# Optimization experiments

Measured on AMD Instinct MI355X. Metric: run time of the kernel, lower is better.

## Reference

```python
import jax, jax.numpy as jnp
import numpy as np

B, T, D, H, NHASH, BS, L, DFF = 4, 4096, 512, 8, 4, 64, 4, 2048
DH = D // H           # 64
NB = T // BS          # 64 buckets per hash round
MASK_VAL = -5e4       # TOKEN_SELF_ATTN_VALUE from reformer-pytorch


def setup_inputs() -> dict:
    key = jax.random.key(0)
    ks = jax.random.split(key, 8)
    s = D ** -0.5
    return {
        "src": jax.random.normal(ks[0], (B, T, D), jnp.float32),
        "rotations": jax.random.normal(ks[1], (L, DH, NHASH, NB // 2), jnp.float32),
        "Wqk": jax.random.normal(ks[2], (L, D, D), jnp.float32) * s,
        "Wv": jax.random.normal(ks[3], (L, D, D), jnp.float32) * s,
        "Wout": jax.random.normal(ks[4], (L, D, D), jnp.float32) * s,
        "bout": jnp.zeros((L, D), jnp.float32),
        "W1": jax.random.normal(ks[5], (L, DFF, D), jnp.float32) * s,
        "b1": jnp.zeros((L, DFF), jnp.float32),
        "W2": jax.random.normal(ks[6], (L, D, DFF), jnp.float32) * (DFF ** -0.5),
        "b2": jnp.zeros((L, D), jnp.float32),
        "g2": jnp.ones((L, D), jnp.float32),
        "be2": jnp.zeros((L, D), jnp.float32),
        "gf": jnp.ones((D,), jnp.float32),
        "bf": jnp.zeros((D,), jnp.float32),
    }


def _ln(x, g, b, eps=1e-6):
    m = x.mean(-1, keepdims=True)
    v = ((x - m) ** 2).mean(-1, keepdims=True)
    return (x - m) * jax.lax.rsqrt(v + eps) * g + b


def _look_one_back(x):
    # concat each chunk with the previous chunk along the within-chunk axis
    return jnp.concatenate([x, jnp.roll(x, 1, axis=1)], axis=2)


def _lsh_attention(qk, v, rot):
    # qk, v: (bh, T, DH); rot: (DH, NHASH, NB//2). Shared-QK LSH attention.
    bh = qk.shape[0]
    rotated = jnp.einsum('btf,fhr->bhtr', qk, rot)               # (bh,NHASH,T,NB/2)
    full = jnp.concatenate([rotated, -rotated], axis=-1)          # (bh,NHASH,T,NB)
    buckets = jnp.argmax(full, axis=-1)                           # (bh,NHASH,T)
    buckets = buckets + (jnp.arange(NHASH) * NB)[None, :, None]   # offset per round
    buckets = buckets.reshape(bh, NHASH * T)

    ticker = jnp.arange(NHASH * T)
    bt = buckets * T + (ticker % T)                               # unique sort keys
    sticker = jnp.argsort(bt, axis=-1)                            # sort positions
    undo = jnp.argsort(sticker, axis=-1)
    st = sticker % T                                              # original positions

    sqk = jnp.take_along_axis(qk, st[..., None], axis=1)          # (bh,NHASH*T,DH)
    sv = jnp.take_along_axis(v, st[..., None], axis=1)

    C = NHASH * NB                                                # chunks
    bq_t = st.reshape(bh, C, BS)
    bqk = sqk.reshape(bh, C, BS, DH)
    bv = sv.reshape(bh, C, BS, DH)

    bq = bqk
    bk = bqk / jnp.maximum(jnp.linalg.norm(bqk, axis=-1, keepdims=True), 1e-12)
    bk = _look_one_back(bk)                                       # (bh,C,2*BS,DH)
    bv = _look_one_back(bv)
    bkv_t = _look_one_back(bq_t)                                  # (bh,C,2*BS)

    dots = jnp.einsum('bcie,bcje->bcij', bq, bk) * (DH ** -0.5)   # (bh,C,BS,2BS)
    self_mask = bq_t[:, :, :, None] == bkv_t[:, :, None, :]
    dots = jnp.where(self_mask, MASK_VAL, dots)

    lse = jax.scipy.special.logsumexp(dots, axis=-1, keepdims=True)
    probs = jnp.exp(dots - lse)
    bo = jnp.einsum('bcij,bcje->bcie', probs, bv)                 # (bh,C,BS,DH)

    so = bo.reshape(bh, NHASH * T, DH)
    slog = lse.reshape(bh, NHASH * T)
    o = jnp.take_along_axis(so, undo[..., None], axis=1).reshape(bh, NHASH, T, DH)
    lg = jnp.take_along_axis(slog, undo, axis=1).reshape(bh, NHASH, T, 1)
    w = jnp.exp(lg - jax.scipy.special.logsumexp(lg, axis=1, keepdims=True))
    return jnp.sum(o * w, axis=1)                                 # (bh,T,DH)


def _split_heads(x):
    return x.reshape(B, T, H, DH).transpose(0, 2, 1, 3).reshape(B * H, T, DH)


def _merge_heads(x):
    return x.reshape(B, H, T, DH).transpose(0, 2, 1, 3).reshape(B, T, D)


def reference(src, rotations, Wqk, Wv, Wout, bout, W1, b1, W2, b2, g2, be2, gf, bf):
    x = src
    for i in range(L):
        # LSH self-attention (post-norm path: norm1 is never applied in source)
        qk = _split_heads(x @ Wqk[i].T)
        v = _split_heads(x @ Wv[i].T)
        att = _merge_heads(_lsh_attention(qk, v, rotations[i]))
        att = att @ Wout[i].T + bout[i]
        x = x + att
        # positionalwise FFN + residual + norm2
        ff = jax.nn.relu(x @ W1[i].T + b1[i]) @ W2[i].T + b2[i]
        x = _ln(x + ff, g2[i], be2[i])
    return _ln(x, gf, bf)
```

## Files before the change

kernel.cpp:

```cpp
#include <hip/hip_runtime.h>
#include <math.h>

#define TT    4096
#define DD    512
#define HH    8
#define DHH   64
#define NH    4
#define LLAY  4
#define DFFN  2048
#define BHH   32
#define NC    256
#define MROWS 16384

typedef __attribute__((ext_vector_type(8))) short s16x8;
typedef __attribute__((ext_vector_type(4))) float f32x4;
typedef unsigned short ushort_t;

union U4 { unsigned u[4]; s16x8 v; };

__device__ __forceinline__ unsigned short f2bf(float f) {
    unsigned u = __float_as_uint(f);
    unsigned r = (u + 0x7FFFu + ((u >> 16) & 1u)) >> 16;
    return (unsigned short)r;
}
__device__ __forceinline__ float bf2f(unsigned short h) {
    return __uint_as_float(((unsigned)h) << 16);
}

__device__ __forceinline__ void xcd_swz(int& bx, int& by) {
    const int gx = gridDim.x;
    const int nwg = gx * gridDim.y;
    const int flat = by * gx + bx;
    const int q = nwg >> 3;
    const int swz = (flat & 7) * q + (flat >> 3);
    bx = swz % gx;
    by = swz / gx;
}

__global__ __launch_bounds__(256) void gemm_bf3_k(
    const ushort_t* __restrict__ Ah, const ushort_t* __restrict__ Al, int lda,
    const ushort_t* __restrict__ Wh, const ushort_t* __restrict__ Wl, int ldw,
    const float* __restrict__ bias, const float* __restrict__ resid,
    float* __restrict__ outf, ushort_t* __restrict__ outh, ushort_t* __restrict__ outl,
    int M, int N, int K, int relu)
{
    __shared__ __align__(16) ushort_t lds[4 * 128 * 32];
    const int tid  = threadIdx.x;
    const int lane = tid & 63;
    const int wv   = tid >> 6;
    const int wm   = wv >> 1, wn = wv & 1;
    int bx = blockIdx.x, by = blockIdx.y;
    xcd_swz(bx, by);
    const int row0 = by * 128, col0 = bx * 128;
    const int g    = lane >> 4;

    f32x4 acc[4][4];
#pragma unroll
    for (int mi = 0; mi < 4; mi++)
#pragma unroll
        for (int ni = 0; ni < 4; ni++) acc[mi][ni] = (f32x4)(0.f);

    const int srow0 = wv * 32;

    for (int k0 = 0; k0 < K; k0 += 32) {
        __syncthreads();
#pragma unroll
        for (int ii = 0; ii < 2; ii++) {
            const int r   = srow0 + ii * 16 + (lane >> 2);
            const int ug  = (((lane & 3) ^ ((r >> 1) & 3)) << 3);
            const size_t ga = (size_t)(row0 + r) * lda + k0 + ug;
            const size_t gw = (size_t)(col0 + r) * ldw + k0 + ug;
            const int lo  = (srow0 + ii * 16) * 32;
            __builtin_amdgcn_global_load_lds(
                (const __attribute__((address_space(1))) void*)(Ah + ga),
                (__attribute__((address_space(3))) void*)&lds[0 * 4096 + lo], 16, 0, 0);
            __builtin_amdgcn_global_load_lds(
                (const __attribute__((address_space(1))) void*)(Al + ga),
                (__attribute__((address_space(3))) void*)&lds[1 * 4096 + lo], 16, 0, 0);
            __builtin_amdgcn_global_load_lds(
                (const __attribute__((address_space(1))) void*)(Wh + gw),
                (__attribute__((address_space(3))) void*)&lds[2 * 4096 + lo], 16, 0, 0);
            __builtin_amdgcn_global_load_lds(
                (const __attribute__((address_space(1))) void*)(Wl + gw),
                (__attribute__((address_space(3))) void*)&lds[3 * 4096 + lo], 16, 0, 0);
        }
        __syncthreads();

        s16x8 ah[4], al[4], wh[4], wl[4];
#pragma unroll
        for (int mi = 0; mi < 4; mi++) {
            const int m  = wm * 64 + mi * 16 + (lane & 15);
            const int pu = ((g ^ ((m >> 1) & 3)) << 3);
            ah[mi] = *(const s16x8*)&lds[0 * 4096 + m * 32 + pu];
            al[mi] = *(const s16x8*)&lds[1 * 4096 + m * 32 + pu];
            const int n  = wn * 64 + mi * 16 + (lane & 15);
            const int pn = ((g ^ ((n >> 1) & 3)) << 3);
            wh[mi] = *(const s16x8*)&lds[2 * 4096 + n * 32 + pn];
            wl[mi] = *(const s16x8*)&lds[3 * 4096 + n * 32 + pn];
        }
#pragma unroll
        for (int mi = 0; mi < 4; mi++)
#pragma unroll
            for (int ni = 0; ni < 4; ni++) {
                acc[mi][ni] = __builtin_amdgcn_mfma_f32_16x16x32_bf16(ah[mi], wh[ni], acc[mi][ni], 0, 0, 0);
                acc[mi][ni] = __builtin_amdgcn_mfma_f32_16x16x32_bf16(al[mi], wh[ni], acc[mi][ni], 0, 0, 0);
                acc[mi][ni] = __builtin_amdgcn_mfma_f32_16x16x32_bf16(ah[mi], wl[ni], acc[mi][ni], 0, 0, 0);
            }
    }

#pragma unroll
    for (int mi = 0; mi < 4; mi++) {
#pragma unroll
        for (int ni = 0; ni < 4; ni++) {
#pragma unroll
            for (int r = 0; r < 4; r++) {
                const int row = row0 + wm * 64 + mi * 16 + g * 4 + r;
                const int col = col0 + wn * 64 + ni * 16 + (lane & 15);
                float v = acc[mi][ni][r];
                if (bias)  v += bias[col];
                if (relu)  v = fmaxf(v, 0.f);
                if (resid) v += resid[(size_t)row * N + col];
                if (outf)  outf[(size_t)row * N + col] = v;
                if (outh) {
                    unsigned short h = f2bf(v);
                    outh[(size_t)row * N + col] = h;
                    outl[(size_t)row * N + col] = f2bf(v - bf2f(h));
                }
            }
        }
    }
}

__global__ __launch_bounds__(256) void gemm_bf6_k(
    const ushort_t* __restrict__ A1, const ushort_t* __restrict__ A2,
    const ushort_t* __restrict__ A3, int lda,
    const ushort_t* __restrict__ W1, const ushort_t* __restrict__ W2,
    const ushort_t* __restrict__ W3,
    float* __restrict__ outf, int M, int N, int K)
{
    __shared__ __align__(16) ushort_t lds[6 * 128 * 32];
    const int tid  = threadIdx.x;
    const int lane = tid & 63;
    const int wv   = tid >> 6;
    const int wm   = wv >> 1, wn = wv & 1;
    int bx = blockIdx.x, by = blockIdx.y;
    xcd_swz(bx, by);
    const int row0 = by * 128, col0 = bx * 128;
    const int g    = lane >> 4;

    f32x4 acc[4][4];
#pragma unroll
    for (int mi = 0; mi < 4; mi++)
#pragma unroll
        for (int ni = 0; ni < 4; ni++) acc[mi][ni] = (f32x4)(0.f);

    const int srow0 = wv * 32;

    for (int k0 = 0; k0 < K; k0 += 32) {
        __syncthreads();
#pragma unroll
        for (int ii = 0; ii < 2; ii++) {
            const int r   = srow0 + ii * 16 + (lane >> 2);
            const int ug  = (((lane & 3) ^ ((r >> 1) & 3)) << 3);
            const size_t ga = (size_t)(row0 + r) * lda + k0 + ug;
            const size_t gw = (size_t)(col0 + r) * K   + k0 + ug;
            const int lo  = (srow0 + ii * 16) * 32;
            __builtin_amdgcn_global_load_lds(
                (const __attribute__((address_space(1))) void*)(A1 + ga),
                (__attribute__((address_space(3))) void*)&lds[0 * 4096 + lo], 16, 0, 0);
            __builtin_amdgcn_global_load_lds(
                (const __attribute__((address_space(1))) void*)(A2 + ga),
                (__attribute__((address_space(3))) void*)&lds[1 * 4096 + lo], 16, 0, 0);
            __builtin_amdgcn_global_load_lds(
                (const __attribute__((address_space(1))) void*)(A3 + ga),
                (__attribute__((address_space(3))) void*)&lds[2 * 4096 + lo], 16, 0, 0);
            __builtin_amdgcn_global_load_lds(
                (const __attribute__((address_space(1))) void*)(W1 + gw),
                (__attribute__((address_space(3))) void*)&lds[3 * 4096 + lo], 16, 0, 0);
            __builtin_amdgcn_global_load_lds(
                (const __attribute__((address_space(1))) void*)(W2 + gw),
                (__attribute__((address_space(3))) void*)&lds[4 * 4096 + lo], 16, 0, 0);
            __builtin_amdgcn_global_load_lds(
                (const __attribute__((address_space(1))) void*)(W3 + gw),
                (__attribute__((address_space(3))) void*)&lds[5 * 4096 + lo], 16, 0, 0);
        }
        __syncthreads();

        s16x8 a1[4], a2[4], a3[4], w1[4], w2[4], w3[4];
#pragma unroll
        for (int mi = 0; mi < 4; mi++) {
            const int m  = wm * 64 + mi * 16 + (lane & 15);
            const int pu = ((g ^ ((m >> 1) & 3)) << 3);
            a1[mi] = *(const s16x8*)&lds[0 * 4096 + m * 32 + pu];
            a2[mi] = *(const s16x8*)&lds[1 * 4096 + m * 32 + pu];
            a3[mi] = *(const s16x8*)&lds[2 * 4096 + m * 32 + pu];
            const int n  = wn * 64 + mi * 16 + (lane & 15);
            const int pn = ((g ^ ((n >> 1) & 3)) << 3);
            w1[mi] = *(const s16x8*)&lds[3 * 4096 + n * 32 + pn];
            w2[mi] = *(const s16x8*)&lds[4 * 4096 + n * 32 + pn];
            w3[mi] = *(const s16x8*)&lds[5 * 4096 + n * 32 + pn];
        }
#pragma unroll
        for (int mi = 0; mi < 4; mi++)
#pragma unroll
            for (int ni = 0; ni < 4; ni++) {
                acc[mi][ni] = __builtin_amdgcn_mfma_f32_16x16x32_bf16(a1[mi], w1[ni], acc[mi][ni], 0, 0, 0);
                acc[mi][ni] = __builtin_amdgcn_mfma_f32_16x16x32_bf16(a2[mi], w1[ni], acc[mi][ni], 0, 0, 0);
                acc[mi][ni] = __builtin_amdgcn_mfma_f32_16x16x32_bf16(a1[mi], w2[ni], acc[mi][ni], 0, 0, 0);
                acc[mi][ni] = __builtin_amdgcn_mfma_f32_16x16x32_bf16(a2[mi], w2[ni], acc[mi][ni], 0, 0, 0);
                acc[mi][ni] = __builtin_amdgcn_mfma_f32_16x16x32_bf16(a1[mi], w3[ni], acc[mi][ni], 0, 0, 0);
                acc[mi][ni] = __builtin_amdgcn_mfma_f32_16x16x32_bf16(a3[mi], w1[ni], acc[mi][ni], 0, 0, 0);
            }
    }

#pragma unroll
    for (int mi = 0; mi < 4; mi++) {
#pragma unroll
        for (int ni = 0; ni < 4; ni++) {
#pragma unroll
            for (int r = 0; r < 4; r++) {
                const int row = row0 + wm * 64 + mi * 16 + g * 4 + r;
                const int col = col0 + wn * 64 + ni * 16 + (lane & 15);
                outf[(size_t)row * N + col] = acc[mi][ni][r];
            }
        }
    }
}

__global__ __launch_bounds__(256) void cvt_k(
    const float* __restrict__ in, ushort_t* __restrict__ o1,
    ushort_t* __restrict__ o2, ushort_t* __restrict__ o3, int n4)
{
    int i = blockIdx.x * 256 + threadIdx.x;
    if (i >= n4) return;
    float4 v = ((const float4*)in)[i];
    float vv[4] = {v.x, v.y, v.z, v.w};
    union { unsigned short us[4]; ushort4 v4; } H, L, M;
#pragma unroll
    for (int q = 0; q < 4; q++) {
        unsigned short a = f2bf(vv[q]);
        float r1 = vv[q] - bf2f(a);
        unsigned short b = f2bf(r1);
        H.us[q] = a; L.us[q] = b;
        M.us[q] = f2bf(r1 - bf2f(b));
    }
    ((ushort4*)o1)[i] = H.v4;
    ((ushort4*)o2)[i] = L.v4;
    if (o3) ((ushort4*)o3)[i] = M.v4;
}

__global__ __launch_bounds__(256) void bucket_k(
    const float* __restrict__ qk, const float* __restrict__ rot,
    int* __restrict__ bkt)
{
    __shared__ float rs[NH][64][32];
    const int bh = blockIdx.y;
    const int t = blockIdx.x * 256 + threadIdx.x;
    for (int i = threadIdx.x; i < NH * 64 * 32; i += 256) {
        int r = i >> 11, f = (i >> 5) & 63, j = i & 31;
        rs[r][f][j] = rot[(f * NH + r) * 32 + j];
    }
    __syncthreads();
    const int b = bh >> 3, h = bh & 7;
    const float* q = qk + ((size_t)(b * TT + t)) * DD + h * DHH;
    float qv[64];
#pragma unroll
    for (int f4 = 0; f4 < 16; f4++) {
        float4 tmp = ((const float4*)q)[f4];
        qv[f4 * 4 + 0] = tmp.x; qv[f4 * 4 + 1] = tmp.y;
        qv[f4 * 4 + 2] = tmp.z; qv[f4 * 4 + 3] = tmp.w;
    }
    for (int r = 0; r < NH; r++) {
        float rv[32];
#pragma unroll
        for (int j = 0; j < 32; j++) rv[j] = 0.f;
        for (int f = 0; f < 64; f++) {
            float qf = qv[f];
#pragma unroll
            for (int j = 0; j < 32; j++) rv[j] = fmaf(qf, rs[r][f][j], rv[j]);
        }
        float best = rv[0];
        int bi = 0;
#pragma unroll
        for (int j = 1; j < 32; j++) { if (rv[j] > best) { best = rv[j]; bi = j; } }
#pragma unroll
        for (int j = 0; j < 32; j++) { float v = -rv[j]; if (v > best) { best = v; bi = 32 + j; } }
        bkt[((size_t)bh * NH + r) * TT + t] = bi;
    }
}

__global__ __launch_bounds__(256) void sort_k(
    const int* __restrict__ bkt, int* __restrict__ st)
{
    __shared__ int lb[TT];
    __shared__ unsigned short cnt[128][64];
    __shared__ int base[64];
    const int r = blockIdx.x, bh = blockIdx.y;
    const int tid = threadIdx.x;
    const int* src = bkt + ((size_t)bh * NH + r) * TT;

    const int4* s4 = (const int4*)src;
    int4* l4 = (int4*)lb;
#pragma unroll
    for (int q = 0; q < 4; q++) l4[tid + q * 256] = s4[tid + q * 256];
    unsigned* cz = (unsigned*)cnt;
#pragma unroll
    for (int q = 0; q < 16; q++) cz[tid + q * 256] = 0;
    __syncthreads();

    if (tid < 128) {
        for (int it = 0; it < 32; it++) {
            int bb = lb[tid * 32 + it];
            cnt[tid][bb]++;
        }
    }
    __syncthreads();

    if (tid < 64) {
        const int bb = tid;
        int run = 0;
        for (int s = 0; s < 128; s++) {
            int t = cnt[s][bb];
            cnt[s][bb] = (unsigned short)run;
            run += t;
        }
        int inc = run;
#pragma unroll
        for (int off = 1; off < 64; off <<= 1) {
            int n = __shfl_up(inc, off, 64);
            if (tid >= off) inc += n;
        }
        base[bb] = inc - run;
    }
    __syncthreads();

    if (tid < 128) {
        int* dst = st + (size_t)bh * (NH * TT) + (size_t)r * TT;
        for (int it = 0; it < 32; it++) {
            int t = tid * 32 + it;
            int bb = lb[t];
            int pos = base[bb] + (int)cnt[tid][bb];
            cnt[tid][bb]++;
            dst[pos] = t;
        }
    }
}

__global__ __launch_bounds__(256, 2) void attn_k(
    const float* __restrict__ qk, const float* __restrict__ vbuf,
    const int* __restrict__ st, float* __restrict__ obuf,
    float* __restrict__ lseb, int bh0)
{
    __shared__ __align__(16) ushort_t ksh[128 * 72];
    __shared__ __align__(16) ushort_t ksl[128 * 72];
    __shared__ __align__(16) unsigned vsp[128 * 66];
    __shared__ float invn[128];
    __shared__ int   tks[128];

    const int c   = blockIdx.x;
    const int bhl = blockIdx.y;
    const int bh  = bh0 + bhl;
    const int b   = bh >> 3, h = bh & 7;
    const int tid = threadIdx.x;
    const int* stb = st + (size_t)bh * (NH * TT);

    if (tid < 128) {
        int cc = (tid < 64) ? c : ((c + NC - 1) & (NC - 1));
        tks[tid] = stb[cc * 64 + (tid & 63)];
    }
    __syncthreads();

    {
        const int row = tid >> 1, c0 = (tid & 1) * 32;
        const int t = tks[row];
        const float4* kg = (const float4*)(qk + ((size_t)(b * TT + t)) * DD + h * DHH + c0);
        const float4* vg = (const float4*)(vbuf + ((size_t)(b * TT + t)) * DD + h * DHH + c0);
        float kv[32], vv[32];
        float ss = 0.f;
#pragma unroll
        for (int q = 0; q < 8; q++) {
            float4 kq = kg[q], vq = vg[q];
            kv[4 * q + 0] = kq.x; kv[4 * q + 1] = kq.y; kv[4 * q + 2] = kq.z; kv[4 * q + 3] = kq.w;
            vv[4 * q + 0] = vq.x; vv[4 * q + 1] = vq.y; vv[4 * q + 2] = vq.z; vv[4 * q + 3] = vq.w;
            ss += kq.x * kq.x + kq.y * kq.y + kq.z * kq.z + kq.w * kq.w;
        }
        ss += __shfl_xor(ss, 1);
        if ((tid & 1) == 0) invn[row] = 1.0f / fmaxf(sqrtf(ss), 1e-12f);

        unsigned hw[16], lw[16];
#pragma unroll
        for (int e = 0; e < 16; e++) {
            float a = kv[2 * e], b2 = kv[2 * e + 1];
            unsigned short ha = f2bf(a), hb = f2bf(b2);
            hw[e] = (unsigned)ha | ((unsigned)hb << 16);
            lw[e] = (unsigned)f2bf(a - bf2f(ha)) | ((unsigned)f2bf(b2 - bf2f(hb)) << 16);
        }
        uint4* kdh = (uint4*)&ksh[row * 72 + c0];
        uint4* kdl = (uint4*)&ksl[row * 72 + c0];
#pragma unroll
        for (int q = 0; q < 4; q++) {
            kdh[q] = make_uint4(hw[4 * q], hw[4 * q + 1], hw[4 * q + 2], hw[4 * q + 3]);
            kdl[q] = make_uint4(lw[4 * q], lw[4 * q + 1], lw[4 * q + 2], lw[4 * q + 3]);
        }
        unsigned pw[32];
#pragma unroll
        for (int e = 0; e < 32; e++) {
            unsigned short hv = f2bf(vv[e]);
            pw[e] = (unsigned)hv | ((unsigned)f2bf(vv[e] - bf2f(hv)) << 16);
        }
        uint2* vd = (uint2*)&vsp[row * 66 + c0];
#pragma unroll
        for (int q = 0; q < 16; q++) vd[q] = make_uint2(pw[2 * q], pw[2 * q + 1]);
    }
    __syncthreads();

    const int lane = tid & 63;
    const int wv   = tid >> 6;
    const int cc16 = lane & 15;
    const int g    = lane >> 4;
    const int rr   = c >> 6;

    f32x4 stt[8];
#pragma unroll
    for (int jt = 0; jt < 8; jt++) stt[jt] = (f32x4)(0.f);

    const int qrow = wv * 16 + cc16;
#pragma unroll
    for (int ks = 0; ks < 2; ks++) {
        s16x8 qh = *(const s16x8*)&ksh[qrow * 72 + ks * 32 + g * 8];
        s16x8 ql = *(const s16x8*)&ksl[qrow * 72 + ks * 32 + g * 8];
#pragma unroll
        for (int jt = 0; jt < 8; jt++) {
            const int krow = jt * 16 + cc16;
            s16x8 ah = *(const s16x8*)&ksh[krow * 72 + ks * 32 + g * 8];
            s16x8 al = *(const s16x8*)&ksl[krow * 72 + ks * 32 + g * 8];
            stt[jt] = __builtin_amdgcn_mfma_f32_16x16x32_bf16(ah, qh, stt[jt], 0, 0, 0);
            stt[jt] = __builtin_amdgcn_mfma_f32_16x16x32_bf16(al, qh, stt[jt], 0, 0, 0);
            stt[jt] = __builtin_amdgcn_mfma_f32_16x16x32_bf16(ah, ql, stt[jt], 0, 0, 0);
        }
    }

    const int tqi = tks[wv * 16 + cc16];
    float m = -INFINITY;
#pragma unroll
    for (int jt = 0; jt < 8; jt++) {
#pragma unroll
        for (int r4 = 0; r4 < 4; r4++) {
            const int j = jt * 16 + g * 4 + r4;
            float d = stt[jt][r4] * invn[j] * 0.125f;
            if (tqi == tks[j]) d = -5e4f;
            stt[jt][r4] = d;
            m = fmaxf(m, d);
        }
    }
    m = fmaxf(m, __shfl_xor(m, 16));
    m = fmaxf(m, __shfl_xor(m, 32));
    float s = 0.f;
#pragma unroll
    for (int jt = 0; jt < 8; jt++) {
#pragma unroll
        for (int r4 = 0; r4 < 4; r4++) {
            float e = expf(stt[jt][r4] - m);
            stt[jt][r4] = e;
            s += e;
        }
    }
    s += __shfl_xor(s, 16);
    s += __shfl_xor(s, 32);
    const float is = 1.0f / s;
    if (g == 0) lseb[((size_t)bh * NH + rr) * TT + tqi] = m + logf(s);

    unsigned ph[8][2], pl[8][2];
#pragma unroll
    for (int jt = 0; jt < 8; jt++) {
#pragma unroll
        for (int w2 = 0; w2 < 2; w2++) {
            float p0 = stt[jt][2 * w2] * is;
            float p1 = stt[jt][2 * w2 + 1] * is;
            unsigned short h0 = f2bf(p0), h1 = f2bf(p1);
            ph[jt][w2] = (unsigned)h0 | ((unsigned)h1 << 16);
            pl[jt][w2] = (unsigned)f2bf(p0 - bf2f(h0)) | ((unsigned)f2bf(p1 - bf2f(h1)) << 16);
        }
    }

    f32x4 occ[4];
#pragma unroll
    for (int nt = 0; nt < 4; nt++) occ[nt] = (f32x4)(0.f);

    const int srcLow  = ((g & 1) << 5) + cc16;
    const int srcHigh = srcLow + 16;
    const bool hiT = (lane & 32) != 0;

#pragma unroll
    for (int ks = 0; ks < 4; ks++) {
        U4 Phi, Plo;
        {
            unsigned a0 = (unsigned)__shfl((int)ph[2 * ks][0], srcLow);
            unsigned a1 = (unsigned)__shfl((int)ph[2 * ks][1], srcLow);
            unsigned a2 = (unsigned)__shfl((int)ph[2 * ks][0], srcHigh);
            unsigned a3 = (unsigned)__shfl((int)ph[2 * ks][1], srcHigh);
            unsigned b0 = (unsigned)__shfl((int)ph[2 * ks + 1][0], srcLow);
            unsigned b1 = (unsigned)__shfl((int)ph[2 * ks + 1][1], srcLow);
            unsigned b2 = (unsigned)__shfl((int)ph[2 * ks + 1][0], srcHigh);
            unsigned b3 = (unsigned)__shfl((int)ph[2 * ks + 1][1], srcHigh);
            Phi.u[0] = hiT ? b0 : a0; Phi.u[1] = hiT ? b1 : a1;
            Phi.u[2] = hiT ? b2 : a2; Phi.u[3] = hiT ? b3 : a3;
            unsigned c0 = (unsigned)__shfl((int)pl[2 * ks][0], srcLow);
            unsigned c1 = (unsigned)__shfl((int)pl[2 * ks][1], srcLow);
            unsigned c2 = (unsigned)__shfl((int)pl[2 * ks][0], srcHigh);
            unsigned c3 = (unsigned)__shfl((int)pl[2 * ks][1], srcHigh);
            unsigned d0 = (unsigned)__shfl((int)pl[2 * ks + 1][0], srcLow);
            unsigned d1 = (unsigned)__shfl((int)pl[2 * ks + 1][1], srcLow);
            unsigned d2 = (unsigned)__shfl((int)pl[2 * ks + 1][0], srcHigh);
            unsigned d3 = (unsigned)__shfl((int)pl[2 * ks + 1][1], srcHigh);
            Plo.u[0] = hiT ? d0 : c0; Plo.u[1] = hiT ? d1 : c1;
            Plo.u[2] = hiT ? d2 : c2; Plo.u[3] = hiT ? d3 : c3;
        }
#pragma unroll
        for (int nt = 0; nt < 4; nt++) {
            unsigned u[8];
#pragma unroll
            for (int e = 0; e < 8; e++)
                u[e] = vsp[(32 * ks + 8 * g + e) * 66 + nt * 16 + cc16];
            U4 Vh, Vl;
#pragma unroll
            for (int m2 = 0; m2 < 4; m2++) {
                Vh.u[m2] = (u[2 * m2] & 0xffffu) | (u[2 * m2 + 1] << 16);
                Vl.u[m2] = (u[2 * m2] >> 16) | (u[2 * m2 + 1] & 0xffff0000u);
            }
            occ[nt] = __builtin_amdgcn_mfma_f32_16x16x32_bf16(Phi.v, Vh.v, occ[nt], 0, 0, 0);
            occ[nt] = __builtin_amdgcn_mfma_f32_16x16x32_bf16(Plo.v, Vh.v, occ[nt], 0, 0, 0);
            occ[nt] = __builtin_amdgcn_mfma_f32_16x16x32_bf16(Phi.v, Vl.v, occ[nt], 0, 0, 0);
        }
    }

#pragma unroll
    for (int r4 = 0; r4 < 4; r4++) {
        const int i = wv * 16 + g * 4 + r4;
        const int ti = tks[i];
        float* dst = obuf + (((size_t)bhl * NH + rr) * TT + ti) * DHH + cc16;
        dst[0]  = occ[0][r4];
        dst[16] = occ[1][r4];
        dst[32] = occ[2][r4];
        dst[48] = occ[3][r4];
    }
}

__global__ __launch_bounds__(256) void combine_k(
    const float* __restrict__ obuf, const float* __restrict__ lseb,
    ushort_t* __restrict__ att, int bh0)
{
    int idx = blockIdx.x * 256 + threadIdx.x;
    int d = idx & 63;
    int t = (idx >> 6) & (TT - 1);
    int bhl = idx >> 18;
    int bh = bh0 + bhl;
    float l0 = lseb[((size_t)bh * NH + 0) * TT + t];
    float l1 = lseb[((size_t)bh * NH + 1) * TT + t];
    float l2 = lseb[((size_t)bh * NH + 2) * TT + t];
    float l3 = lseb[((size_t)bh * NH + 3) * TT + t];
    float m = fmaxf(fmaxf(l0, l1), fmaxf(l2, l3));
    float e0 = expf(l0 - m), e1 = expf(l1 - m), e2 = expf(l2 - m), e3 = expf(l3 - m);
    float inv = 1.0f / (e0 + e1 + e2 + e3);
    float o0 = obuf[(((size_t)bhl * NH + 0) * TT + t) * DHH + d];
    float o1 = obuf[(((size_t)bhl * NH + 1) * TT + t) * DHH + d];
    float o2 = obuf[(((size_t)bhl * NH + 2) * TT + t) * DHH + d];
    float o3 = obuf[(((size_t)bhl * NH + 3) * TT + t) * DHH + d];
    float o = (e0 * o0 + e1 * o1 + e2 * o2 + e3 * o3) * inv;
    int b = bh >> 3, h = bh & 7;
    size_t base = (size_t)(b * TT + t) * 1024 + h * DHH + d;
    unsigned short hi = f2bf(o);
    att[base]       = hi;
    att[base + 512] = f2bf(o - bf2f(hi));
}

__global__ __launch_bounds__(64) void ln_k(
    const float* __restrict__ in, const float* __restrict__ g,
    const float* __restrict__ be, float* __restrict__ out,
    ushort_t* __restrict__ oh, ushort_t* __restrict__ ol,
    ushort_t* __restrict__ ol2)
{
    const int row = blockIdx.x;
    const int tid = threadIdx.x;
    const float* x = in + (size_t)row * DD;
    float4 a = *(const float4*)(x + tid * 8);
    float4 b = *(const float4*)(x + tid * 8 + 4);
    float s = a.x + a.y + a.z + a.w + b.x + b.y + b.z + b.w;
#pragma unroll
    for (int o = 32; o >= 1; o >>= 1) s += __shfl_xor(s, o, 64);
    float mean = s * (1.0f / 512.0f);
    float dx[8];
    dx[0] = a.x - mean; dx[1] = a.y - mean; dx[2] = a.z - mean; dx[3] = a.w - mean;
    dx[4] = b.x - mean; dx[5] = b.y - mean; dx[6] = b.z - mean; dx[7] = b.w - mean;
    float ss = 0.f;
#pragma unroll
    for (int q = 0; q < 8; q++) ss += dx[q] * dx[q];
#pragma unroll
    for (int o = 32; o >= 1; o >>= 1) ss += __shfl_xor(ss, o, 64);
    float var = ss * (1.0f / 512.0f);
    float inv = 1.0f / sqrtf(var + 1e-6f);
    const float* gp = g + tid * 8;
    const float* bp = be + tid * 8;
    float y[8];
#pragma unroll
    for (int q = 0; q < 8; q++) y[q] = dx[q] * inv * gp[q] + bp[q];
    float* yp = out + (size_t)row * DD + tid * 8;
    *(float4*)(yp)     = make_float4(y[0], y[1], y[2], y[3]);
    *(float4*)(yp + 4) = make_float4(y[4], y[5], y[6], y[7]);
    if (oh) {
        union { unsigned short us[8]; ushort4 v4[2]; } H, L, M;
#pragma unroll
        for (int q = 0; q < 8; q++) {
            unsigned short h = f2bf(y[q]);
            float r1 = y[q] - bf2f(h);
            unsigned short l = f2bf(r1);
            H.us[q] = h; L.us[q] = l;
            M.us[q] = f2bf(r1 - bf2f(l));
        }
        size_t e = (size_t)row * DD + tid * 8;
        *(ushort4*)(oh + e)      = H.v4[0];
        *(ushort4*)(oh + e + 4)  = H.v4[1];
        *(ushort4*)(ol + e)      = L.v4[0];
        *(ushort4*)(ol + e + 4)  = L.v4[1];
        *(ushort4*)(ol2 + e)     = M.v4[0];
        *(ushort4*)(ol2 + e + 4) = M.v4[1];
    }
}

extern "C" void kernel_launch(void* const* d_in, const int* in_sizes, int n_in,
                              void* d_out, int out_size, void* d_ws, size_t ws_size,
                              hipStream_t stream)
{
    const float* src  = (const float*)d_in[0];
    const float* rots = (const float*)d_in[1];
    const float* Wqk  = (const float*)d_in[2];
    const float* Wv   = (const float*)d_in[3];
    const float* Wout = (const float*)d_in[4];
    const float* bout = (const float*)d_in[5];
    const float* W1   = (const float*)d_in[6];
    const float* b1   = (const float*)d_in[7];
    const float* W2   = (const float*)d_in[8];
    const float* b2   = (const float*)d_in[9];
    const float* g2   = (const float*)d_in[10];
    const float* be2  = (const float*)d_in[11];
    const float* gf   = (const float*)d_in[12];
    const float* bf   = (const float*)d_in[13];
    float* out = (float*)d_out;

    char* w = (char*)d_ws;
    const size_t SZ_X = (size_t)MROWS * DD * 4;
    const size_t XHALF = (size_t)MROWS * DD;
    float*    x     = (float*)(w);
    ushort_t* xs    = (ushort_t*)(w + SZ_X);
    ushort_t* xh    = xs;
    ushort_t* xl    = xs + XHALF;
    ushort_t* xl2   = xs + 2 * XHALF;
    char*     p     = w + SZ_X + 3 * XHALF * 2;
    float*    qkb   = (float*)(p);
    ushort_t* attb  = (ushort_t*)(p);
    float*    vb    = (float*)(p + SZ_X);
    float*    obuf  = (float*)(p + 2 * SZ_X);
    ushort_t* h1b   = (ushort_t*)(p + 2 * SZ_X);
    ushort_t* wb    = (ushort_t*)(p + 4 * SZ_X);
    char*     tail  = p + 4 * SZ_X + 6029312 * 2;
    int*      bkt   = (int*)(tail);
    int*      st    = (int*)(tail + (size_t)BHH * NH * TT * 4);
    float*    lseb  = (float*)(tail + 2 * (size_t)BHH * NH * TT * 4);

    ushort_t* wvh = wb;            ushort_t* wvl = wb + 262144;
    ushort_t* woh = wb + 524288;   ushort_t* wol = wb + 786432;
    ushort_t* w1h = wb + 1048576;  ushort_t* w1l = wb + 2097152;
    ushort_t* w2h = wb + 3145728;  ushort_t* w2l = wb + 4194304;
    ushort_t* wq1 = wb + 5242880;  ushort_t* wq2 = wb + 5505024;
    ushort_t* wq3 = wb + 5767168;
    const size_t H1HALF = (size_t)MROWS * 1024;
    ushort_t* h1h = h1b;           ushort_t* h1l = h1b + H1HALF;

    hipMemcpyAsync(x, src, SZ_X, hipMemcpyDeviceToDevice, stream);
    cvt_k<<<(MROWS * DD / 4 + 255) / 256, 256, 0, stream>>>(src, xh, xl, xl2, MROWS * DD / 4);

    for (int i = 0; i < LLAY; i++) {
        const float* Wqk_i = Wqk + (size_t)i * DD * DD;
        const float* Wv_i  = Wv  + (size_t)i * DD * DD;
        const float* Wout_i= Wout+ (size_t)i * DD * DD;
        const float* bout_i= bout+ (size_t)i * DD;
        const float* W1_i  = W1  + (size_t)i * DFFN * DD;
        const float* b1_i  = b1  + (size_t)i * DFFN;
        const float* W2_i  = W2  + (size_t)i * DD * DFFN;
        const float* b2_i  = b2  + (size_t)i * DD;
        const float* g2_i  = g2  + (size_t)i * DD;
        const float* be2_i = be2 + (size_t)i * DD;
        const float* rot_i = rots + (size_t)i * DHH * NH * 32;

        cvt_k<<<(262144 / 4 + 255) / 256, 256, 0, stream>>>(Wqk_i, wq1, wq2, wq3, 262144 / 4);
        cvt_k<<<(262144 / 4 + 255) / 256, 256, 0, stream>>>(Wv_i, wvh, wvl, nullptr, 262144 / 4);
        cvt_k<<<(262144 / 4 + 255) / 256, 256, 0, stream>>>(Wout_i, woh, wol, nullptr, 262144 / 4);
        cvt_k<<<(1048576 / 4 + 255) / 256, 256, 0, stream>>>(W1_i, w1h, w1l, nullptr, 1048576 / 4);
        cvt_k<<<(1048576 / 4 + 255) / 256, 256, 0, stream>>>(W2_i, w2h, w2l, nullptr, 1048576 / 4);

        gemm_bf6_k<<<dim3(4, 128), 256, 0, stream>>>(xh, xl, xl2, DD, wq1, wq2, wq3,
                                                     qkb, MROWS, DD, DD);
        gemm_bf3_k<<<dim3(4, 128), 256, 0, stream>>>(xh, xl, DD, wvh, wvl, DD,
                                                     nullptr, nullptr, vb, nullptr, nullptr,
                                                     MROWS, DD, DD, 0);
        bucket_k<<<dim3(16, BHH), 256, 0, stream>>>(qkb, rot_i, bkt);
        sort_k<<<dim3(NH, BHH), 256, 0, stream>>>(bkt, st);

        for (int s = 0; s < 2; s++) {
            attn_k<<<dim3(NC, 16), 256, 0, stream>>>(qkb, vb, st, obuf, lseb, s * 16);
            combine_k<<<16384, 256, 0, stream>>>(obuf, lseb, attb, s * 16);
        }

        gemm_bf3_k<<<dim3(4, 128), 256, 0, stream>>>(attb, attb + 512, 1024, woh, wol, DD,
                                                     bout_i, x, x, xh, xl,
                                                     MROWS, DD, DD, 0);
        for (int hf = 0; hf < 2; hf++) {
            const size_t wo = (size_t)hf * 1024;
            gemm_bf3_k<<<dim3(8, 128), 256, 0, stream>>>(xh, xl, DD,
                                                         w1h + wo * DD, w1l + wo * DD, DD,
                                                         b1_i + wo, nullptr,
                                                         nullptr, h1h, h1l,
                                                         MROWS, 1024, DD, 1);
            gemm_bf3_k<<<dim3(4, 128), 256, 0, stream>>>(h1h, h1l, 1024,
                                                         w2h + wo, w2l + wo, DFFN,
                                                         hf == 0 ? b2_i : nullptr,
                                                         hf == 0 ? x : vb,
                                                         vb, nullptr, nullptr,
                                                         MROWS, DD, 1024, 0);
        }
        ln_k<<<MROWS, 64, 0, stream>>>(vb, g2_i, be2_i, x, xh, xl, xl2);
    }
    ln_k<<<MROWS, 64, 0, stream>>>(x, gf, bf, out, nullptr, nullptr, nullptr);
}
```

Before: 3.212 ms.

## Double-buffer LDS tiles in bf16x3 GEMM to overlap loads with MFMA

Splits the GEMM's shared-memory staging into two buffers and issues the next K-tile's global-to-LDS loads before computing on the current tile, with explicit vmcnt waits and barriers. This hides global load latency behind the MFMA work. It doubles the LDS footprint to 64KB per block, which may lower occupancy. It also depends on the hand-set vmcnt count matching the number of outstanding loads.

```diff
diff --git a/kernel.cpp b/kernel.cpp
--- a/kernel.cpp
+++ b/kernel.cpp
@@ -44,7 +44,7 @@
     float* __restrict__ outf, ushort_t* __restrict__ outh, ushort_t* __restrict__ outl,
     int M, int N, int K, int relu)
 {
-    __shared__ __align__(16) ushort_t lds[4 * 128 * 32];
+    __shared__ __align__(16) ushort_t lds[2][4 * 128 * 32];
     const int tid  = threadIdx.x;
     const int lane = tid & 63;
     const int wv   = tid >> 6;
@@ -53,6 +53,7 @@
     xcd_swz(bx, by);
     const int row0 = by * 128, col0 = bx * 128;
     const int g    = lane >> 4;
+    const int srow0 = wv * 32;
 
     f32x4 acc[4][4];
 #pragma unroll
@@ -60,10 +61,7 @@
 #pragma unroll
         for (int ni = 0; ni < 4; ni++) acc[mi][ni] = (f32x4)(0.f);
 
-    const int srow0 = wv * 32;
-
-    for (int k0 = 0; k0 < K; k0 += 32) {
-        __syncthreads();
+    auto STAGE = [&](int buf, int k0) {
 #pragma unroll
         for (int ii = 0; ii < 2; ii++) {
             const int r   = srow0 + ii * 16 + (lane >> 2);
@@ -73,30 +71,44 @@
             const int lo  = (srow0 + ii * 16) * 32;
             __builtin_amdgcn_global_load_lds(
                 (const __attribute__((address_space(1))) void*)(Ah + ga),
-                (__attribute__((address_space(3))) void*)&lds[0 * 4096 + lo], 16, 0, 0);
+                (__attribute__((address_space(3))) void*)&lds[buf][0 * 4096 + lo], 16, 0, 0);
             __builtin_amdgcn_global_load_lds(
                 (const __attribute__((address_space(1))) void*)(Al + ga),
-                (__attribute__((address_space(3))) void*)&lds[1 * 4096 + lo], 16, 0, 0);
+                (__attribute__((address_space(3))) void*)&lds[buf][1 * 4096 + lo], 16, 0, 0);
             __builtin_amdgcn_global_load_lds(
                 (const __attribute__((address_space(1))) void*)(Wh + gw),
-                (__attribute__((address_space(3))) void*)&lds[2 * 4096 + lo], 16, 0, 0);
+                (__attribute__((address_space(3))) void*)&lds[buf][2 * 4096 + lo], 16, 0, 0);
             __builtin_amdgcn_global_load_lds(
                 (const __attribute__((address_space(1))) void*)(Wl + gw),
-                (__attribute__((address_space(3))) void*)&lds[3 * 4096 + lo], 16, 0, 0);
-        }
-        __syncthreads();
+                (__attribute__((address_space(3))) void*)&lds[buf][3 * 4096 + lo], 16, 0, 0);
+        }
+    };
+
+    const int nt = K >> 5;
+    STAGE(0, 0);
+
+    for (int t = 0; t < nt; ++t) {
+        const int cur = t & 1;
+        if (t + 1 < nt) {
+            STAGE(cur ^ 1, (t + 1) << 5);
+            asm volatile("s_waitcnt vmcnt(8)" ::: "memory");
+        } else {
+            asm volatile("s_waitcnt vmcnt(0)" ::: "memory");
+        }
+        __builtin_amdgcn_s_barrier();
+        __builtin_amdgcn_sched_barrier(0);
 
         s16x8 ah[4], al[4], wh[4], wl[4];
 #pragma unroll
         for (int mi = 0; mi < 4; mi++) {
             const int m  = wm * 64 + mi * 16 + (lane & 15);
             const int pu = ((g ^ ((m >> 1) & 3)) << 3);
-            ah[mi] = *(const s16x8*)&lds[0 * 4096 + m * 32 + pu];
-            al[mi] = *(const s16x8*)&lds[1 * 4096 + m * 32 + pu];
+            ah[mi] = *(const s16x8*)&lds[cur][0 * 4096 + m * 32 + pu];
+            al[mi] = *(const s16x8*)&lds[cur][1 * 4096 + m * 32 + pu];
             const int n  = wn * 64 + mi * 16 + (lane & 15);
             const int pn = ((g ^ ((n >> 1) & 3)) << 3);
-            wh[mi] = *(const s16x8*)&lds[2 * 4096 + n * 32 + pn];
-            wl[mi] = *(const s16x8*)&lds[3 * 4096 + n * 32 + pn];
+            wh[mi] = *(const s16x8*)&lds[cur][2 * 4096 + n * 32 + pn];
+            wl[mi] = *(const s16x8*)&lds[cur][3 * 4096 + n * 32 + pn];
         }
 #pragma unroll
         for (int mi = 0; mi < 4; mi++)
@@ -106,6 +118,9 @@
                 acc[mi][ni] = __builtin_amdgcn_mfma_f32_16x16x32_bf16(al[mi], wh[ni], acc[mi][ni], 0, 0, 0);
                 acc[mi][ni] = __builtin_amdgcn_mfma_f32_16x16x32_bf16(ah[mi], wl[ni], acc[mi][ni], 0, 0, 0);
             }
+
+        __builtin_amdgcn_sched_barrier(0);
+        __builtin_amdgcn_s_barrier();
     }
 
 #pragma unroll
```

Result: faster. 3.111 ms (-3.2%).
